# Kernel tuning notes

Measured on AMD Instinct MI355X. Metric: run time of the kernel, lower is better.

Reference implementation:

```python
import jax, jax.numpy as jnp
import numpy as np

EPS = 1e-7  # K.epsilon()


def setup_inputs() -> dict:
    key = jax.random.key(0)
    k1, k2, k3 = jax.random.split(key, 3)
    B, H, W, Cin, Cout, KH, KW = 8, 128, 128, 256, 256, 3, 3
    x = jax.random.normal(k1, (B, H, W, Cin), dtype=jnp.float32)
    style = jax.random.normal(k2, (B, Cin), dtype=jnp.float32)
    # he_uniform-ish scale for the kernel
    fan_in = KH * KW * Cin
    limit = np.sqrt(6.0 / fan_in)
    kernel = jax.random.uniform(k3, (KH, KW, Cin, Cout), dtype=jnp.float32,
                                minval=-limit, maxval=limit)
    return {"x": x, "style": style, "kernel": kernel}


def reference(x, style, kernel):
    # Demodulation factor: rsqrt(sum_{kh,kw,cin} (kernel * style)^2 + eps), shape (B, Cout).
    # Equivalent to the original's broadcast-then-reduce, computed without
    # materializing the (B,kh,kw,Cin,Cout) modulated weight tensor.
    k2 = jnp.sum(jnp.square(kernel), axis=(0, 1))          # (Cin, Cout)
    ssq = jnp.einsum('io,bi->bo', k2, jnp.square(style))   # (B, Cout)
    demod = jax.lax.rsqrt(ssq + EPS)                       # (B, Cout)

    # Modulate input per-sample, then shared-weight conv (same padding, stride 1).
    xm = x * style[:, None, None, :]                       # (B,H,W,Cin)
    y = jax.lax.conv_general_dilated(
        xm, kernel,
        window_strides=(1, 1), padding='SAME',
        dimension_numbers=('NHWC', 'HWIO', 'NHWC'))
    return y * demod[:, None, None, :]
```

## Files before the change

kernel.cpp:

```cpp
#include <hip/hip_runtime.h>
#include <hip/hip_bf16.h>
#include <stdint.h>

typedef short short8 __attribute__((ext_vector_type(8)));
typedef float f32x4 __attribute__((ext_vector_type(4)));

__device__ __forceinline__ short f2bf(float f) {
    __hip_bfloat16 h = __float2bfloat16(f);
    return __builtin_bit_cast(short, h);
}

__global__ void prep_xm(const float* __restrict__ x,
                        const float* __restrict__ style,
                        __hip_bfloat16* __restrict__ xm)
{
    const size_t gi = ((size_t)blockIdx.x * 256 + threadIdx.x) * 8;
    const int b  = (int)(gi >> 22);
    const int ci = (int)(gi & 255);
    float4 x0 = *(const float4*)(x + gi);
    float4 x1 = *(const float4*)(x + gi + 4);
    float4 s0 = *(const float4*)(style + b * 256 + ci);
    float4 s1 = *(const float4*)(style + b * 256 + ci + 4);
    short8 m;
#pragma unroll
    for (int jj = 0; jj < 4; ++jj) {
        m[jj]     = f2bf((&x0.x)[jj] * (&s0.x)[jj]);
        m[jj + 4] = f2bf((&x1.x)[jj] * (&s1.x)[jj]);
    }
    *(short8*)(xm + gi) = m;
}

__global__ void prep_k2(const float* __restrict__ kern, float* __restrict__ K2)
{
    const int ci = blockIdx.x, co = threadIdx.x;
    float acc = 0.f;
#pragma unroll
    for (int p = 0; p < 9; ++p) {
        float w = kern[(p * 256 + ci) * 256 + co];
        acc += w * w;
    }
    K2[ci * 256 + co] = acc;
}

__global__ void prep_demod(const float* __restrict__ style,
                           const float* __restrict__ K2,
                           float* __restrict__ demod)
{
    const int b = blockIdx.x, co = threadIdx.x;
    __shared__ float s2[256];
    float s = style[b * 256 + co];
    s2[co] = s * s;
    __syncthreads();
    float acc = 0.f;
#pragma unroll 8
    for (int ci = 0; ci < 256; ++ci)
        acc += s2[ci] * K2[ci * 256 + co];
    demod[b * 256 + co] = 1.0f / sqrtf(acc + 1e-7f);
}

__global__ void prep_kf(const float* __restrict__ kern,
                        __hip_bfloat16* __restrict__ kf)
{
    const int st = blockIdx.x;
    const int sl = st / 3, tp = st - sl * 3;
    const int dh = sl >> 3, cc = sl & 7;
    const int p  = dh * 3 + tp;
    const int t    = threadIdx.x;
    const int lane = t & 63, jt2 = t >> 6;
    const int l15  = lane & 15, lk = lane >> 4;
    const int cib  = cc * 32 + lk * 8;
#pragma unroll
    for (int jj = 0; jj < 4; ++jj) {
        const int jt = jj * 4 + jt2;
        const int co = jt * 16 + l15;
        short8 v;
#pragma unroll
        for (int e = 0; e < 8; ++e)
            v[e] = f2bf(kern[(size_t)(p * 256 + cib + e) * 256 + co]);
        *(short8*)(kf + ((size_t)(st * 16 + jt) * 64 + lane) * 8) = v;
    }
}

__global__ __launch_bounds__(256) void conv_mfma(
    const __hip_bfloat16* __restrict__ xm,
    const __hip_bfloat16* __restrict__ kf,
    const float* __restrict__ demod,
    float* __restrict__ out)
{
    __shared__ __align__(16) __hip_bfloat16 Xs[2][130 * 32];
    __shared__ __align__(16) __hip_bfloat16 KfB[2][24 * 512];
    __shared__ float Ds[128];

    const int t    = threadIdx.x;
    const int bid  = blockIdx.x;
    const int L    = ((bid & 7) << 8) | (bid >> 3);
    const int n0   = (L & 1) << 7;
    const int bh   = L >> 1;
    const int b    = bh >> 7, h = bh & 127;
    const int wave = t >> 6, lane = t & 63;
    const int wr   = (wave >> 1) << 6;
    const int wc   = (wave & 1) << 6;
    const int wjl  = (wave & 1) << 2;
    const int l15  = lane & 15, lk = lane >> 4;
    const int jb0  = (L & 1) << 3;

    if (t < 128) Ds[t] = demod[b * 256 + n0 + t];
    if (t < 32) {
        const __hip_bfloat16 z = __float2bfloat16(0.f);
        Xs[0][t] = z; Xs[0][129 * 32 + t] = z;
        Xs[1][t] = z; Xs[1][129 * 32 + t] = z;
    }

    f32x4 acc[4][4] = {};

    const int slo = (h == 0)   ? 8  : 0;
    const int shi = (h == 127) ? 16 : 24;

    auto stage_A = [&](int s, int buf) {
        const int h2  = h + (s >> 3) - 1;
        const int ci0 = (s & 7) << 5;
        const size_t rowbase = (size_t)(b * 128 + h2) * 128;
        const int lr = lane >> 2, slot = lane & 3;
#pragma unroll
        for (int k = 0; k < 2; ++k) {
            const int d = (wave << 1) | k;
            const int r = 1 + (d << 4) + lr;
            const int c = slot ^ ((r >> 1) & 3);
            const __hip_bfloat16* src =
                xm + (rowbase + (r - 1)) * 256 + ci0 + (c << 3);
            __builtin_amdgcn_global_load_lds(
                (const __attribute__((address_space(1))) void*)src,
                (__attribute__((address_space(3))) void*)&Xs[buf][(1 + (d << 4)) * 32],
                16, 0, 0);
        }
    };
    auto stage_B = [&](int s, int buf) {
#pragma unroll
        for (int k = 0; k < 6; ++k) {
            const int c = (k << 2) + wave;
            const __hip_bfloat16* src =
                kf + ((size_t)(s * 48 + ((c >> 3) << 4) + jb0 + (c & 7)) * 64
                      + lane) * 8;
            __builtin_amdgcn_global_load_lds(
                (const __attribute__((address_space(1))) void*)src,
                (__attribute__((address_space(3))) void*)&KfB[buf][c * 512],
                16, 0, 0);
        }
    };

    stage_A(slo, 0);
    stage_B(slo, 0);
    __syncthreads();

    int cur = 0;
    for (int s = slo; s < shi; ++s, cur ^= 1) {
        if (s + 1 < shi) {
            stage_A(s + 1, cur ^ 1);
            stage_B(s + 1, cur ^ 1);
        }

#pragma unroll
        for (int tp = 0; tp < 3; ++tp) {
            short8 af[4], bfr[4];
#pragma unroll
            for (int j = 0; j < 4; ++j)
                bfr[j] = *(const short8*)&KfB[cur][((tp << 3) + wjl + j) * 512
                                                   + lane * 8];
#pragma unroll
            for (int i = 0; i < 4; ++i) {
                const int R = wr + i * 16 + l15 + tp;
                af[i] = *(const short8*)&Xs[cur][R * 32
                                                 + ((lk ^ ((R >> 1) & 3)) << 3)];
            }
#pragma unroll
            for (int i = 0; i < 4; ++i)
#pragma unroll
                for (int j = 0; j < 4; ++j)
                    acc[i][j] = __builtin_amdgcn_mfma_f32_16x16x32_bf16(
                        af[i], bfr[j], acc[i][j], 0, 0, 0);
        }
        __syncthreads();
    }

    float dj[4];
#pragma unroll
    for (int j = 0; j < 4; ++j) dj[j] = Ds[wc + j * 16 + l15];
    const size_t obase = (size_t)(b * 128 + h) * 128 * 256 + n0;
#pragma unroll
    for (int i = 0; i < 4; ++i) {
#pragma unroll
        for (int j = 0; j < 4; ++j) {
            const int n = wc + j * 16 + l15;
#pragma unroll
            for (int r = 0; r < 4; ++r) {
                const int m = wr + i * 16 + (lane >> 4) * 4 + r;
                out[obase + (size_t)m * 256 + n] = acc[i][j][r] * dj[j];
            }
        }
    }
}

extern "C" void kernel_launch(void* const* d_in, const int* in_sizes, int n_in,
                              void* d_out, int out_size, void* d_ws, size_t ws_size,
                              hipStream_t stream)
{
    const float* x     = (const float*)d_in[0];
    const float* style = (const float*)d_in[1];
    const float* kern  = (const float*)d_in[2];
    float* out = (float*)d_out;

    char* ws = (char*)d_ws;
    __hip_bfloat16* xm = (__hip_bfloat16*)ws;
    float* demod = (float*)(ws + 67108864);
    float* K2    = (float*)(ws + 67108864 + 8192);
    __hip_bfloat16* kT = (__hip_bfloat16*)(ws + 67108864 + 270336);

    prep_xm   <<<16384, 256, 0, stream>>>(x, style, xm);
    prep_k2   <<<256,   256, 0, stream>>>(kern, K2);
    prep_demod<<<8,     256, 0, stream>>>(style, K2, demod);
    prep_kf   <<<72,    256, 0, stream>>>(kern, kT);
    conv_mfma <<<2048,  256, 0, stream>>>(xm, kT, demod, out);
}
```

Measured before the change: 370.9 us.

## Load conv weight fragments directly to registers and unroll pipeline by two

The conv kernel no longer stages the weight fragments through LDS. Each wave loads its 12 B fragments per stage straight from global memory into a register double-buffer (B0/B1). The stage loop is unrolled by two with static buffer indices, and scheduling barriers keep the loads ahead of the MFMA compute. The change also adds an occupancy hint of 2 blocks per CU and makes prep_xm process 16 elements per thread. The aim is to cut LDS traffic and LDS footprint, at the cost of higher register pressure and more redundant global and L2 reads of the weights. The unrolled loop assumes an even stage count, which holds for the ranges 8..24, 0..16 and 0..24.

```diff
diff --git a/kernel.cpp b/kernel.cpp
--- a/kernel.cpp
+++ b/kernel.cpp
@@ -10,24 +10,28 @@
     return __builtin_bit_cast(short, h);
 }
 
-__global__ void prep_xm(const float* __restrict__ x,
+__global__ __launch_bounds__(256) void prep_xm(const float* __restrict__ x,
                         const float* __restrict__ style,
                         __hip_bfloat16* __restrict__ xm)
 {
-    const size_t gi = ((size_t)blockIdx.x * 256 + threadIdx.x) * 8;
+    const size_t gi = ((size_t)blockIdx.x * 256 + threadIdx.x) * 16;
     const int b  = (int)(gi >> 22);
     const int ci = (int)(gi & 255);
-    float4 x0 = *(const float4*)(x + gi);
-    float4 x1 = *(const float4*)(x + gi + 4);
-    float4 s0 = *(const float4*)(style + b * 256 + ci);
-    float4 s1 = *(const float4*)(style + b * 256 + ci + 4);
-    short8 m;
-#pragma unroll
-    for (int jj = 0; jj < 4; ++jj) {
-        m[jj]     = f2bf((&x0.x)[jj] * (&s0.x)[jj]);
-        m[jj + 4] = f2bf((&x1.x)[jj] * (&s1.x)[jj]);
-    }
-    *(short8*)(xm + gi) = m;
+    const float* sp = style + b * 256 + ci;
+#pragma unroll
+    for (int half = 0; half < 2; ++half) {
+        float4 x0 = *(const float4*)(x + gi + half * 8);
+        float4 x1 = *(const float4*)(x + gi + half * 8 + 4);
+        float4 s0 = *(const float4*)(sp + half * 8);
+        float4 s1 = *(const float4*)(sp + half * 8 + 4);
+        short8 m;
+#pragma unroll
+        for (int jj = 0; jj < 4; ++jj) {
+            m[jj]     = f2bf((&x0.x)[jj] * (&s0.x)[jj]);
+            m[jj + 4] = f2bf((&x1.x)[jj] * (&s1.x)[jj]);
+        }
+        *(short8*)(xm + gi + half * 8) = m;
+    }
 }
 
 __global__ void prep_k2(const float* __restrict__ kern, float* __restrict__ K2)
@@ -81,14 +85,13 @@
     }
 }
 
-__global__ __launch_bounds__(256) void conv_mfma(
+__global__ __launch_bounds__(256, 2) void conv_mfma(
     const __hip_bfloat16* __restrict__ xm,
     const __hip_bfloat16* __restrict__ kf,
     const float* __restrict__ demod,
     float* __restrict__ out)
 {
     __shared__ __align__(16) __hip_bfloat16 Xs[2][130 * 32];
-    __shared__ __align__(16) __hip_bfloat16 KfB[2][24 * 512];
     __shared__ float Ds[128];
 
     const int t    = threadIdx.x;
@@ -100,9 +103,8 @@
     const int wave = t >> 6, lane = t & 63;
     const int wr   = (wave >> 1) << 6;
     const int wc   = (wave & 1) << 6;
-    const int wjl  = (wave & 1) << 2;
     const int l15  = lane & 15, lk = lane >> 4;
-    const int jb0  = (L & 1) << 3;
+    const int jt0  = ((L & 1) << 3) + ((wave & 1) << 2);
 
     if (t < 128) Ds[t] = demod[b * 256 + n0 + t];
     if (t < 32) {
@@ -134,42 +136,24 @@
                 16, 0, 0);
         }
     };
-    auto stage_B = [&](int s, int buf) {
-#pragma unroll
-        for (int k = 0; k < 6; ++k) {
-            const int c = (k << 2) + wave;
-            const __hip_bfloat16* src =
-                kf + ((size_t)(s * 48 + ((c >> 3) << 4) + jb0 + (c & 7)) * 64
-                      + lane) * 8;
-            __builtin_amdgcn_global_load_lds(
-                (const __attribute__((address_space(1))) void*)src,
-                (__attribute__((address_space(3))) void*)&KfB[buf][c * 512],
-                16, 0, 0);
-        }
+
+    auto load_B = [&](int s, short8 (&B)[12]) {
+#pragma unroll
+        for (int tp = 0; tp < 3; ++tp)
+#pragma unroll
+            for (int j = 0; j < 4; ++j)
+                B[tp * 4 + j] = *(const short8*)(kf +
+                    ((size_t)(s * 48 + tp * 16 + jt0 + j) * 64 + lane) * 8);
     };
 
-    stage_A(slo, 0);
-    stage_B(slo, 0);
-    __syncthreads();
-
-    int cur = 0;
-    for (int s = slo; s < shi; ++s, cur ^= 1) {
-        if (s + 1 < shi) {
-            stage_A(s + 1, cur ^ 1);
-            stage_B(s + 1, cur ^ 1);
-        }
-
+    auto compute = [&](int buf, const short8 (&B)[12]) {
 #pragma unroll
         for (int tp = 0; tp < 3; ++tp) {
-            short8 af[4], bfr[4];
-#pragma unroll
-            for (int j = 0; j < 4; ++j)
-                bfr[j] = *(const short8*)&KfB[cur][((tp << 3) + wjl + j) * 512
-                                                   + lane * 8];
+            short8 af[4];
 #pragma unroll
             for (int i = 0; i < 4; ++i) {
                 const int R = wr + i * 16 + l15 + tp;
-                af[i] = *(const short8*)&Xs[cur][R * 32
+                af[i] = *(const short8*)&Xs[buf][R * 32
                                                  + ((lk ^ ((R >> 1) & 3)) << 3)];
             }
 #pragma unroll
@@ -177,8 +161,29 @@
 #pragma unroll
                 for (int j = 0; j < 4; ++j)
                     acc[i][j] = __builtin_amdgcn_mfma_f32_16x16x32_bf16(
-                        af[i], bfr[j], acc[i][j], 0, 0, 0);
-        }
+                        af[i], B[tp * 4 + j], acc[i][j], 0, 0, 0);
+        }
+    };
+
+    short8 B0[12], B1[12];
+
+    stage_A(slo, 0);
+    load_B(slo, B0);
+    __syncthreads();
+
+    for (int s = slo; s < shi; s += 2) {
+        stage_A(s + 1, 1);
+        load_B(s + 1, B1);
+        __builtin_amdgcn_sched_barrier(0);
+        compute(0, B0);
+        __syncthreads();
+
+        if (s + 2 < shi) {
+            stage_A(s + 2, 0);
+            load_B(s + 2, B0);
+        }
+        __builtin_amdgcn_sched_barrier(0);
+        compute(1, B1);
         __syncthreads();
     }
 
@@ -193,7 +198,7 @@
             const int n = wc + j * 16 + l15;
 #pragma unroll
             for (int r = 0; r < 4; ++r) {
-                const int m = wr + i * 16 + (lane >> 4) * 4 + r;
+                const int m = wr + i * 16 + lk * 4 + r;
                 out[obase + (size_t)m * 256 + n] = acc[i][j][r] * dj[j];
             }
         }
@@ -215,9 +220,9 @@
     float* K2    = (float*)(ws + 67108864 + 8192);
     __hip_bfloat16* kT = (__hip_bfloat16*)(ws + 67108864 + 270336);
 
-    prep_xm   <<<16384, 256, 0, stream>>>(x, style, xm);
-    prep_k2   <<<256,   256, 0, stream>>>(kern, K2);
-    prep_demod<<<8,     256, 0, stream>>>(style, K2, demod);
-    prep_kf   <<<72,    256, 0, stream>>>(kern, kT);
-    conv_mfma <<<2048,  256, 0, stream>>>(xm, kT, demod, out);
-}
+    prep_xm   <<<8192, 256, 0, stream>>>(x, style, xm);
+    prep_k2   <<<256,  256, 0, stream>>>(kern, K2);
+    prep_demod<<<8,    256, 0, stream>>>(style, K2, demod);
+    prep_kf   <<<72,   256, 0, stream>>>(kern, kT);
+    conv_mfma <<<2048, 256, 0, stream>>>(xm, kT, demod, out);
+}
```

Result: no change. 373.0 us (+0.6%).
